# Performance work log

Hardware: AMD Instinct MI355X
Metric: run time of the kernel (lower is better)

Reference implementation:

```python
import jax, jax.numpy as jnp
import numpy as np
from jax import lax

NUM_EXPERTS = 5
K = 3


def setup_inputs() -> dict:
    key = jax.random.key(0)
    ks = jax.random.split(key, 16)
    B = 8192
    d_in, d_h = 32 * 10 * 10, 128

    def w(k, shape, fan_in):
        return jax.random.normal(k, shape, jnp.float32) / np.sqrt(fan_in)

    return {
        "x": jax.random.normal(ks[0], (B, 1, 28, 28), jnp.float32),
        # conv feature extractor: 28 -> conv5 -> 24 -> pool2 -> 12 -> conv3 -> 10
        "conv1_w": w(ks[1], (16, 1, 5, 5), 25),
        "conv1_b": jnp.zeros((16,), jnp.float32),
        "conv2_w": w(ks[2], (32, 16, 3, 3), 16 * 9),
        "conv2_b": jnp.zeros((32,), jnp.float32),
        # top-k gate
        "gate_w": w(ks[3], (d_in, NUM_EXPERTS), d_in),
        "gate_b": jnp.zeros((NUM_EXPERTS,), jnp.float32),
        # 5 experts: Linear(3200,128)-Tanh-Linear(128,128)-Tanh, stacked on axis 0
        "e1_w": w(ks[4], (NUM_EXPERTS, d_in, d_h), d_in),
        "e1_b": jnp.zeros((NUM_EXPERTS, d_h), jnp.float32),
        "e2_w": w(ks[5], (NUM_EXPERTS, d_h, d_h), d_h),
        "e2_b": jnp.zeros((NUM_EXPERTS, d_h), jnp.float32),
        # softmax head
        "sm_w": w(ks[6], (d_h, 10), d_h),
        "sm_b": jnp.zeros((10,), jnp.float32),
    }


def _conv_features(x, c1w, c1b, c2w, c2b):
    dn = ("NCHW", "OIHW", "NCHW")
    h = lax.conv_general_dilated(x, c1w, (1, 1), "VALID", dimension_numbers=dn)
    h = jax.nn.relu(h + c1b[None, :, None, None])          # [B,16,24,24]
    h = lax.reduce_window(h, -jnp.inf, lax.max, (1, 1, 2, 2), (1, 1, 2, 2), "VALID")  # [B,16,12,12]
    h = lax.conv_general_dilated(h, c2w, (1, 1), "VALID", dimension_numbers=dn)
    h = jax.nn.relu(h + c2b[None, :, None, None])          # [B,32,10,10]
    return h.reshape(h.shape[0], -1)                       # [B,3200]


def reference(x, conv1_w, conv1_b, conv2_w, conv2_b, gate_w, gate_b,
              e1_w, e1_b, e2_w, e2_b, sm_w, sm_b):
    h = _conv_features(x, conv1_w, conv1_b, conv2_w, conv2_b)  # [B, 3200]
    B = h.shape[0]

    # token-choice top-K gating over NUM_EXPERTS experts
    probs = jax.nn.softmax(h @ gate_w + gate_b, axis=-1)       # [B, E]
    topv, topi = lax.top_k(probs, K)                           # [B, K]
    topv = topv / jnp.sum(topv, axis=-1, keepdims=True)        # renormalize
    w_full = jnp.zeros((B, NUM_EXPERTS), h.dtype).at[
        jnp.arange(B)[:, None], topi].set(topv)                # [B, E] sparse combine weights

    # expert MLPs (small, computed densely and masked by gate weights)
    h1 = jnp.tanh(jnp.einsum("bd,edh->ebh", h, e1_w) + e1_b[:, None, :])   # [E,B,128]
    h2 = jnp.tanh(jnp.einsum("ebh,ehk->ebk", h1, e2_w) + e2_b[:, None, :])  # [E,B,128]
    moe_out = jnp.einsum("be,ebk->bk", w_full, h2)             # weighted sum combine, [B,128]

    logits = moe_out @ sm_w + sm_b                             # [B,10]
    return jax.nn.softmax(logits, axis=1)
```

## Files before the change

### kernel.cpp

```cpp
#include <hip/hip_runtime.h>
#include <hip/hip_bf16.h>
#include <hip/hip_fp16.h>

#define NB 8192
#define D_IN 3200
#define D_H 128
#define NE 5

typedef _Float16 f16x8 __attribute__((ext_vector_type(8)));
typedef _Float16 f16x4 __attribute__((ext_vector_type(4)));
typedef float f32x4 __attribute__((ext_vector_type(4)));

__device__ __forceinline__ void gload16(const _Float16* g, _Float16* l) {
    __builtin_amdgcn_global_load_lds(
        (const __attribute__((address_space(1))) void*)g,
        (__attribute__((address_space(3))) void*)l, 16, 0, 0);
}

__global__ __launch_bounds__(256) void k_gwprep(const float* __restrict__ gw,
                                                float* __restrict__ gwC,
                                                int* __restrict__ cnt) {
    int i = blockIdx.x * 256 + threadIdx.x;
    if (i < 16000) {
        int e = i / 3200, rem = i - e * 3200;
        int o = rem >> 5, co = rem & 31;
        gwC[i] = gw[(co * 100 + o) * 5 + e];
    }
    if (blockIdx.x == 0 && threadIdx.x < NE) cnt[threadIdx.x] = 0;
}

#define PCL_S 24
__global__ __launch_bounds__(256, 3) void k_feat(
    const float* __restrict__ x, const float* __restrict__ c1w, const float* __restrict__ c1b,
    const float* __restrict__ c2w, const float* __restrict__ c2b,
    const float* __restrict__ gwC, const float* __restrict__ gb,
    const float* __restrict__ e1w, _Float16* __restrict__ wT,
    const float* __restrict__ e2w, _Float16* __restrict__ e2T,
    _Float16* __restrict__ h16, float* __restrict__ wfull)
{
    __shared__ union {
        struct {
            __align__(16) float xs[784];
            __align__(16) float c1wsP[448];
            __align__(16) _Float16 b2h[5120];
            __align__(16) _Float16 b2l[5120];
            __align__(16) _Float16 pclh[144 * PCL_S];
            __align__(16) _Float16 pcll[144 * PCL_S];
            float red[32];
        } f;
        float tile[64 * 65];
    } S;
    int bid = blockIdx.x;
    int t = threadIdx.x;

    if (bid < 520) {
        if (bid < 500) {
            int e = bid / 100, rem = bid - e * 100;
            int k0 = (rem >> 1) * 64, n0 = (rem & 1) * 64;
            const float* src = e1w + (size_t)e * D_IN * D_H;
            _Float16* dst = wT + (size_t)e * D_H * D_IN;
            for (int i = 0; i < 16; ++i) {
                int idx = t + i * 256;
                int kr = idx >> 6, nc = idx & 63;
                S.tile[kr * 65 + nc] = src[(size_t)(k0 + kr) * D_H + n0 + nc];
            }
            __syncthreads();
            for (int i = 0; i < 16; ++i) {
                int idx = t + i * 256;
                int nr = idx >> 6, kc = idx & 63;
                dst[(size_t)(n0 + nr) * D_IN + k0 + kc] = (_Float16)S.tile[kc * 65 + nr];
            }
        } else {
            int idx2 = bid - 500;
            int e = idx2 >> 2, rem = idx2 & 3;
            int k0 = (rem >> 1) * 64, n0 = (rem & 1) * 64;
            const float* src = e2w + (size_t)e * D_H * D_H;
            _Float16* dst = e2T + (size_t)e * D_H * D_H;
            for (int i = 0; i < 16; ++i) {
                int idx = t + i * 256;
                int kr = idx >> 6, nc = idx & 63;
                S.tile[kr * 65 + nc] = src[(size_t)(k0 + kr) * D_H + n0 + nc];
            }
            __syncthreads();
            for (int i = 0; i < 16; ++i) {
                int idx = t + i * 256;
                int nr = idx >> 6, kc = idx & 63;
                dst[(size_t)(n0 + nr) * D_H + k0 + kc] = (_Float16)S.tile[kc * 65 + nr];
            }
        }
        return;
    }

    int b = bid - 520;
    for (int i = t; i < 784; i += 256) S.f.xs[i] = x[(size_t)b * 784 + i];
    for (int i = t; i < 400; i += 256) {
        int c = i / 25, q = i - c * 25;
        S.f.c1wsP[c * 28 + q] = c1w[i];
    }
    for (int i = t; i < 5120; i += 256) {
        int co = i / 160, k = i - co * 160;
        int s = k >> 4, ci = k & 15;
        float v = (s == 9) ? 0.f : c2w[(co * 16 + ci) * 9 + s];
        _Float16 vh = (_Float16)v;
        S.f.b2h[i] = vh;
        S.f.b2l[i] = (_Float16)(v - (float)vh);
    }
    __syncthreads();

    {
        int c = t >> 4;
        int tile = t & 15;
        int tr = tile >> 2, tc = tile & 3;
        float w1r[25];
        #pragma unroll
        for (int q = 0; q < 6; ++q) {
            float4 v4 = *(const float4*)&S.f.c1wsP[c * 28 + q * 4];
            w1r[q * 4 + 0] = v4.x; w1r[q * 4 + 1] = v4.y;
            w1r[q * 4 + 2] = v4.z; w1r[q * 4 + 3] = v4.w;
        }
        w1r[24] = S.f.c1wsP[c * 28 + 24];
        float bias1 = c1b[c];
        float win[5][10];
        float pacc[3][3];
        #pragma unroll
        for (int i = 0; i < 3; ++i)
            #pragma unroll
            for (int j = 0; j < 3; ++j) pacc[i][j] = 0.f;
        int r0 = 6 * tr, col0 = 6 * tc;
        #pragma unroll
        for (int cr = 0; cr < 6; ++cr) {
            if (cr == 0) {
                #pragma unroll
                for (int rr = 0; rr < 5; ++rr)
                    #pragma unroll
                    for (int m = 0; m < 5; ++m) {
                        float2 v = *(const float2*)&S.f.xs[(r0 + rr) * 28 + col0 + 2 * m];
                        win[rr][2 * m] = v.x; win[rr][2 * m + 1] = v.y;
                    }
            } else {
                int dstr = (cr + 4) % 5;
                #pragma unroll
                for (int m = 0; m < 5; ++m) {
                    float2 v = *(const float2*)&S.f.xs[(r0 + cr + 4) * 28 + col0 + 2 * m];
                    win[dstr][2 * m] = v.x; win[dstr][2 * m + 1] = v.y;
                }
            }
            #pragma unroll
            for (int oc = 0; oc < 6; ++oc) {
                float s = bias1;
                #pragma unroll
                for (int u = 0; u < 5; ++u)
                    #pragma unroll
                    for (int v = 0; v < 5; ++v)
                        s += win[(cr + u) % 5][oc + v] * w1r[u * 5 + v];
                s = fmaxf(s, 0.f);
                pacc[cr >> 1][oc >> 1] = fmaxf(pacc[cr >> 1][oc >> 1], s);
            }
        }
        #pragma unroll
        for (int i = 0; i < 3; ++i)
            #pragma unroll
            for (int j = 0; j < 3; ++j) {
                int pos = (3 * tr + i) * 12 + (3 * tc + j);
                float v = pacc[i][j];
                _Float16 vh = (_Float16)v;
                S.f.pclh[pos * PCL_S + c] = vh;
                S.f.pcll[pos * PCL_S + c] = (_Float16)(v - (float)vh);
            }
    }
    __syncthreads();

    float part[5] = {0, 0, 0, 0, 0};
    int lane = t & 63, wv = t >> 6;
    int quad = lane >> 4, l16 = lane & 15;
    int quadh = quad >> 1, quadl = quad & 1;
    const int offA[5] = {0, 2, 13, 24, 26};
    const int offB[5] = {1, 12, 14, 25, 0};
    {
        int nt = wv & 1;
        int co = nt * 16 + l16;
        f16x8 bh[5], bl[5];
        #pragma unroll
        for (int kc = 0; kc < 5; ++kc) {
            bh[kc] = *(const f16x8*)&S.f.b2h[co * 160 + kc * 32 + quad * 8];
            bl[kc] = *(const f16x8*)&S.f.b2l[co * 160 + kc * 32 + quad * 8];
        }
        float bco = c2b[co];
        for (int mt = wv >> 1; mt < 7; mt += 2) {
            int o_a = mt * 16 + l16;
            int o_cl = o_a < 100 ? o_a : 99;
            int pb = (o_cl / 10) * 12 + (o_cl % 10);
            f32x4 acc = (f32x4){0.f, 0.f, 0.f, 0.f};
            #pragma unroll
            for (int kc = 0; kc < 5; ++kc) {
                int off = quadh ? offB[kc] : offA[kc];
                f16x8 ah = *(const f16x8*)&S.f.pclh[(pb + off) * PCL_S + quadl * 8];
                f16x8 al = *(const f16x8*)&S.f.pcll[(pb + off) * PCL_S + quadl * 8];
                acc = __builtin_amdgcn_mfma_f32_16x16x32_f16(ah, bh[kc], acc, 0, 0, 0);
                acc = __builtin_amdgcn_mfma_f32_16x16x32_f16(ah, bl[kc], acc, 0, 0, 0);
                acc = __builtin_amdgcn_mfma_f32_16x16x32_f16(al, bh[kc], acc, 0, 0, 0);
            }
            if (mt < 6 || quad == 0) {
                int o0 = mt * 16 + quad * 4;
                f16x4 st;
                #pragma unroll
                for (int r = 0; r < 4; ++r) {
                    float hv = fmaxf(acc[r] + bco, 0.f);
                    st[r] = (_Float16)hv;
                    #pragma unroll
                    for (int e = 0; e < 5; ++e)
                        part[e] += hv * gwC[e * 3200 + (o0 + r) * 32 + co];
                }
                *(f16x4*)&h16[(size_t)b * D_IN + co * 100 + o0] = st;
            }
        }
    }

    #pragma unroll
    for (int e = 0; e < 5; ++e) {
        float v = part[e];
        for (int off = 32; off > 0; off >>= 1) v += __shfl_down(v, off, 64);
        if (lane == 0) S.f.red[wv * 8 + e] = v;
    }
    __syncthreads();
    if (t == 0) {
        float lg[5], p[5];
        float mx = -1e30f;
        for (int e = 0; e < 5; ++e) {
            lg[e] = S.f.red[e] + S.f.red[8 + e] + S.f.red[16 + e] + S.f.red[24 + e] + gb[e];
            mx = fmaxf(mx, lg[e]);
        }
        float sum = 0.f;
        for (int e = 0; e < 5; ++e) { p[e] = expf(lg[e] - mx); sum += p[e]; }
        for (int e = 0; e < 5; ++e) p[e] /= sum;
        bool used[5] = {false, false, false, false, false};
        float out5[5] = {0, 0, 0, 0, 0};
        int ti[3]; float tv[3]; float tsum = 0.f;
        for (int jj = 0; jj < 3; ++jj) {
            int best = 0; float bv = -1.f;
            for (int e = 0; e < 5; ++e)
                if (!used[e] && p[e] > bv) { bv = p[e]; best = e; }
            used[best] = true; ti[jj] = best; tv[jj] = bv; tsum += bv;
        }
        for (int jj = 0; jj < 3; ++jj) out5[ti[jj]] = tv[jj] / tsum;
        for (int e = 0; e < 5; ++e) wfull[b * 5 + e] = out5[e];
    }
}

__global__ __launch_bounds__(256) void k_compact(
    const float* __restrict__ wfull, int* __restrict__ cnt, int* __restrict__ lists)
{
    int tok = blockIdx.x * 256 + threadIdx.x;
    int lane = threadIdx.x & 63;
    float w[5];
    #pragma unroll
    for (int e = 0; e < 5; ++e) w[e] = wfull[(size_t)tok * 5 + e];
    #pragma unroll
    for (int e = 0; e < 5; ++e) {
        bool sel = w[e] > 0.f;
        unsigned long long mask = __ballot(sel);
        int leader = __ffsll((long long)mask) - 1;
        int base = 0;
        if (lane == leader) base = atomicAdd(&cnt[e], __popcll(mask));
        base = __shfl(base, leader, 64);
        if (sel) {
            int pos = base + __popcll(mask & ((1ull << lane) - 1ull));
            lists[e * NB + pos] = tok;
        }
    }
}

#define H1S 136
union __align__(16) SLds {
    struct { _Float16 As0[2048], As1[2048], Bs0[4096], Bs1[4096]; } p[2];
    struct {
        __align__(16) _Float16 h1s[64 * H1S];
        __align__(16) _Float16 e2ws[128 * H1S];
    } q;
};

__global__ __launch_bounds__(256, 3) void k_e1e2(
    const _Float16* __restrict__ h16, const _Float16* __restrict__ wT,
    const _Float16* __restrict__ e2T,
    const float* __restrict__ e1b, const float* __restrict__ e2b,
    const float* __restrict__ smw,
    const float* __restrict__ wfull, const int* __restrict__ cnt,
    const int* __restrict__ lists, float* __restrict__ logits)
{
    __shared__ SLds u;
    __shared__ float wfl[64];
    __shared__ int rows[64];
    int bid = blockIdx.x;
    int e = bid >> 7;
    int mt = bid & 127;
    int cnt_e = cnt[e];
    int m0 = mt * 64;
    if (m0 >= cnt_e) return;
    int t = threadIdx.x;
    int lane = t & 63, wv = t >> 6;
    int waveM = wv >> 1, waveN = wv & 1;
    int quad = lane >> 4, l16 = lane & 15;
    if (t < 64) {
        int r = m0 + t;
        int row = (r < cnt_e) ? lists[e * NB + r] : lists[e * NB];
        rows[t] = row;
        wfl[t] = (r < cnt_e) ? wfull[(size_t)row * 5 + e] : 0.f;
    }
    __syncthreads();

    const _Float16* bbase = wT + (size_t)e * (D_H * D_IN);
    int srow = t >> 2;
    int scol = (t & 3) * 8;
    const _Float16* aptr = h16 + (size_t)rows[srow] * D_IN + scol;
    const _Float16* bptr0 = bbase + (size_t)srow * D_IN + scol;
    const _Float16* bptr1 = bbase + (size_t)(64 + srow) * D_IN + scol;
    f32x4 acc[2][4];
    #pragma unroll
    for (int i = 0; i < 2; ++i)
        #pragma unroll
        for (int j = 0; j < 4; ++j) acc[i][j] = (f32x4){0.f, 0.f, 0.f, 0.f};

    _Float16* bufc = (_Float16*)&u.p[0];
    _Float16* bufn = (_Float16*)&u.p[1];
    #define STAGE(base, kk)                                           \
        do {                                                          \
            gload16(aptr  + (kk),        (base) + 0    + wv * 512);   \
            gload16(aptr  + (kk) + 32,   (base) + 2048 + wv * 512);   \
            gload16(bptr0 + (kk),        (base) + 4096 + wv * 512);   \
            gload16(bptr0 + (kk) + 32,   (base) + 8192 + wv * 512);   \
            gload16(bptr1 + (kk),        (base) + 4096 + 2048 + wv * 512); \
            gload16(bptr1 + (kk) + 32,   (base) + 8192 + 2048 + wv * 512); \
        } while (0)

    STAGE(bufc, 0);
    const int NT = D_IN / 64;
    for (int it = 0; it < NT; ++it) {
        if (it + 1 < NT) {
            STAGE(bufn, (it + 1) * 64);
            asm volatile("s_waitcnt vmcnt(6)" ::: "memory");
        } else {
            asm volatile("s_waitcnt vmcnt(0)" ::: "memory");
        }
        __builtin_amdgcn_s_barrier();
        __builtin_amdgcn_sched_barrier(0);
        #pragma unroll
        for (int ch = 0; ch < 2; ++ch) {
            const _Float16* Ab = bufc + (ch ? 2048 : 0);
            const _Float16* Bb = bufc + 4096 + (ch ? 4096 : 0);
            f16x8 af[2], bf[4];
            #pragma unroll
            for (int ms = 0; ms < 2; ++ms)
                af[ms] = *(const f16x8*)&Ab[(waveM * 32 + ms * 16 + l16) * 32 + quad * 8];
            #pragma unroll
            for (int ns = 0; ns < 4; ++ns)
                bf[ns] = *(const f16x8*)&Bb[(waveN * 64 + ns * 16 + l16) * 32 + quad * 8];
            #pragma unroll
            for (int ms = 0; ms < 2; ++ms)
                #pragma unroll
                for (int ns = 0; ns < 4; ++ns)
                    acc[ms][ns] = __builtin_amdgcn_mfma_f32_16x16x32_f16(af[ms], bf[ns], acc[ms][ns], 0, 0, 0);
        }
        __builtin_amdgcn_s_barrier();
        _Float16* tmp = bufc; bufc = bufn; bufn = tmp;
    }
    #undef STAGE

    #pragma unroll
    for (int ms = 0; ms < 2; ++ms) {
        int rbase = waveM * 32 + ms * 16 + quad * 4;
        #pragma unroll
        for (int ns = 0; ns < 4; ++ns) {
            int n = waveN * 64 + ns * 16 + l16;
            float bias = e1b[e * D_H + n];
            #pragma unroll
            for (int r = 0; r < 4; ++r)
                u.q.h1s[(rbase + r) * H1S + n] = (_Float16)tanhf(acc[ms][ns][r] + bias);
        }
    }
    __syncthreads();

    {
        int rr = t >> 1, cc = (t & 1) * 64;
        const _Float16* src = e2T + (size_t)e * (D_H * D_H) + (size_t)rr * D_H + cc;
        #pragma unroll
        for (int i = 0; i < 8; ++i)
            *(uint4*)&u.q.e2ws[rr * H1S + cc + i * 8] = *(const uint4*)(src + i * 8);
    }
    __syncthreads();

    f32x4 acc2[2][4];
    #pragma unroll
    for (int i = 0; i < 2; ++i)
        #pragma unroll
        for (int j = 0; j < 4; ++j) acc2[i][j] = (f32x4){0.f, 0.f, 0.f, 0.f};
    #pragma unroll
    for (int kc = 0; kc < 4; ++kc) {
        f16x8 a2[2], b2[4];
        #pragma unroll
        for (int ms = 0; ms < 2; ++ms)
            a2[ms] = *(const f16x8*)&u.q.h1s[(waveM * 32 + ms * 16 + l16) * H1S + kc * 32 + quad * 8];
        #pragma unroll
        for (int ns = 0; ns < 4; ++ns)
            b2[ns] = *(const f16x8*)&u.q.e2ws[(waveN * 64 + ns * 16 + l16) * H1S + kc * 32 + quad * 8];
        #pragma unroll
        for (int ms = 0; ms < 2; ++ms)
            #pragma unroll
            for (int ns = 0; ns < 4; ++ns)
                acc2[ms][ns] = __builtin_amdgcn_mfma_f32_16x16x32_f16(a2[ms], b2[ns], acc2[ms][ns], 0, 0, 0);
    }
    __syncthreads();

    _Float16* smwT = u.q.e2ws;
    for (int i = t; i < 2048; i += 256) {
        int n = i >> 7, k = i & 127;
        smwT[i] = (_Float16)(n < 10 ? smw[k * 10 + n] : 0.f);
    }
    #pragma unroll
    for (int ms = 0; ms < 2; ++ms) {
        int rbase = waveM * 32 + ms * 16 + quad * 4;
        #pragma unroll
        for (int ns = 0; ns < 4; ++ns) {
            int n = waveN * 64 + ns * 16 + l16;
            float bias = e2b[e * D_H + n];
            #pragma unroll
            for (int r = 0; r < 4; ++r) {
                int lrow = rbase + r;
                u.q.h1s[lrow * H1S + n] = (_Float16)(wfl[lrow] * tanhf(acc2[ms][ns][r] + bias));
            }
        }
    }
    __syncthreads();

    {
        f32x4 acc3 = (f32x4){0.f, 0.f, 0.f, 0.f};
        #pragma unroll
        for (int kc = 0; kc < 4; ++kc) {
            f16x8 a3 = *(const f16x8*)&u.q.h1s[(wv * 16 + l16) * H1S + kc * 32 + quad * 8];
            f16x8 b3 = *(const f16x8*)&smwT[l16 * 128 + kc * 32 + quad * 8];
            acc3 = __builtin_amdgcn_mfma_f32_16x16x32_f16(a3, b3, acc3, 0, 0, 0);
        }
        if (l16 < 10) {
            #pragma unroll
            for (int r = 0; r < 4; ++r) {
                int row = wv * 16 + quad * 4 + r;
                unsafeAtomicAdd(&logits[(size_t)rows[row] * 10 + l16], acc3[r]);
            }
        }
    }
}

__global__ __launch_bounds__(256) void k_smax(
    const float* __restrict__ logits, const float* __restrict__ smb,
    float* __restrict__ out)
{
    int r = blockIdx.x * 256 + threadIdx.x;
    float lg[10];
    float mx = -1e30f;
    #pragma unroll
    for (int c = 0; c < 10; ++c) {
        lg[c] = logits[(size_t)r * 10 + c] + smb[c];
        mx = fmaxf(mx, lg[c]);
    }
    float s = 0.f;
    #pragma unroll
    for (int c = 0; c < 10; ++c) { lg[c] = expf(lg[c] - mx); s += lg[c]; }
    float inv = 1.f / s;
    #pragma unroll
    for (int c = 0; c < 10; ++c) out[(size_t)r * 10 + c] = lg[c] * inv;
}

extern "C" void kernel_launch(void* const* d_in, const int* in_sizes, int n_in,
                              void* d_out, int out_size, void* d_ws, size_t ws_size,
                              hipStream_t stream)
{
    const float* x   = (const float*)d_in[0];
    const float* c1w = (const float*)d_in[1];
    const float* c1b = (const float*)d_in[2];
    const float* c2w = (const float*)d_in[3];
    const float* c2b = (const float*)d_in[4];
    const float* gw  = (const float*)d_in[5];
    const float* gb  = (const float*)d_in[6];
    const float* e1w = (const float*)d_in[7];
    const float* e1b = (const float*)d_in[8];
    const float* e2w = (const float*)d_in[9];
    const float* e2b = (const float*)d_in[10];
    const float* smw = (const float*)d_in[11];
    const float* smb = (const float*)d_in[12];
    float* out = (float*)d_out;

    char* ws = (char*)d_ws;
    size_t off = 0;
    auto alloc = [&](size_t bytes) {
        void* p = ws + off;
        off += (bytes + 255) & ~(size_t)255;
        return p;
    };
    _Float16* h16 = (_Float16*)alloc((size_t)NB * D_IN * 2);
    _Float16* wT  = (_Float16*)alloc((size_t)NE * D_H * D_IN * 2);
    _Float16* e2T = (_Float16*)alloc((size_t)NE * D_H * D_H * 2);
    float* wfull  = (float*)alloc((size_t)NB * NE * 4);
    float* logits = (float*)alloc((size_t)NB * 10 * 4);
    float* gwC    = (float*)alloc((size_t)NE * D_IN * 4);
    int* cnt      = (int*)alloc(NE * 4);
    int* lists    = (int*)alloc((size_t)NE * NB * 4);

    hipMemsetAsync(logits, 0, (size_t)NB * 10 * 4, stream);
    k_gwprep<<<dim3(63), 256, 0, stream>>>(gw, gwC, cnt);
    k_feat<<<dim3(520 + NB), 256, 0, stream>>>(x, c1w, c1b, c2w, c2b, gwC, gb,
                                               e1w, wT, e2w, e2T, h16, wfull);
    k_compact<<<dim3(NB / 256), 256, 0, stream>>>(wfull, cnt, lists);
    k_e1e2<<<dim3(128 * NE), 256, 0, stream>>>(h16, wT, e2T, e1b, e2b, smw,
                                               wfull, cnt, lists, logits);
    k_smax<<<dim3(NB / 256), 256, 0, stream>>>(logits, smb, out);
}
```

Measured before the change: 304.8 us.

## Run conv1 on MFMA with split-fp16 and precompute packed conv weights

Conv1 plus maxpool moves from a scalar FP32 sliding-window loop to MFMA 16x16x32 f16 instructions. Inputs and weights are split into hi/lo fp16 pairs and three MFMAs per tile recover near-fp32 accuracy. The conv2 and conv1 weight split/packing now happens once in the prep kernel, and each block copies the packed weights into LDS with direct global-to-LDS loads instead of recomputing them per block. LDS use shrinks enough that launch bounds rise to 4 blocks per SM, at some accuracy risk from dropping the lo*lo term.

```diff
diff --git a/kernel.cpp b/kernel.cpp
--- a/kernel.cpp
+++ b/kernel.cpp
@@ -17,33 +17,63 @@
         (__attribute__((address_space(3))) void*)l, 16, 0, 0);
 }
 
-__global__ __launch_bounds__(256) void k_gwprep(const float* __restrict__ gw,
-                                                float* __restrict__ gwC,
-                                                int* __restrict__ cnt) {
+__device__ __forceinline__ unsigned pack_hl(float v) {
+    _Float16 vh = (_Float16)v;
+    _Float16 vl = (_Float16)(v - (float)vh);
+    unsigned short uh, ul;
+    __builtin_memcpy(&uh, &vh, 2);
+    __builtin_memcpy(&ul, &vl, 2);
+    return (unsigned)uh | ((unsigned)ul << 16);
+}
+
+__global__ __launch_bounds__(256) void k_prep(const float* __restrict__ gw,
+                                              const float* __restrict__ c2w,
+                                              const float* __restrict__ c1w,
+                                              float* __restrict__ gwC,
+                                              _Float16* __restrict__ wpk,
+                                              int* __restrict__ cnt) {
     int i = blockIdx.x * 256 + threadIdx.x;
     if (i < 16000) {
         int e = i / 3200, rem = i - e * 3200;
         int o = rem >> 5, co = rem & 31;
         gwC[i] = gw[(co * 100 + o) * 5 + e];
+    } else if (i < 21120) {
+        int j = i - 16000;
+        int co = j / 160, k = j - co * 160;
+        int s = k >> 4, ci = k & 15;
+        float v = (s == 9) ? 0.f : c2w[(co * 16 + ci) * 9 + s];
+        _Float16 vh = (_Float16)v;
+        wpk[j] = vh;
+        wpk[5120 + j] = (_Float16)(v - (float)vh);
+    } else if (i < 21760) {
+        int j = i - 21120;
+        int c = (j * 1639) >> 16;
+        int k = j - c * 40;
+        float v = (k < 25) ? c1w[c * 25 + k] : 0.f;
+        _Float16 vh = (_Float16)v;
+        wpk[10240 + j] = vh;
+        wpk[10880 + j] = (_Float16)(v - (float)vh);
     }
     if (blockIdx.x == 0 && threadIdx.x < NE) cnt[threadIdx.x] = 0;
 }
 
 #define PCL_S 24
-__global__ __launch_bounds__(256, 3) void k_feat(
-    const float* __restrict__ x, const float* __restrict__ c1w, const float* __restrict__ c1b,
-    const float* __restrict__ c2w, const float* __restrict__ c2b,
+__global__ __launch_bounds__(256, 4) void k_feat(
+    const float* __restrict__ x, const float* __restrict__ c1b,
+    const float* __restrict__ c2b,
     const float* __restrict__ gwC, const float* __restrict__ gb,
+    const _Float16* __restrict__ wpk,
     const float* __restrict__ e1w, _Float16* __restrict__ wT,
     const float* __restrict__ e2w, _Float16* __restrict__ e2T,
     _Float16* __restrict__ h16, float* __restrict__ wfull)
 {
     __shared__ union {
         struct {
-            __align__(16) float xs[784];
-            __align__(16) float c1wsP[448];
             __align__(16) _Float16 b2h[5120];
             __align__(16) _Float16 b2l[5120];
+            __align__(16) _Float16 b1h[640];
+            __align__(16) _Float16 b1l[640];
+            __align__(16) unsigned xs_hl[784];
             __align__(16) _Float16 pclh[144 * PCL_S];
             __align__(16) _Float16 pcll[144 * PCL_S];
             float red[32];
@@ -92,87 +122,63 @@
     }
 
     int b = bid - 520;
-    for (int i = t; i < 784; i += 256) S.f.xs[i] = x[(size_t)b * 784 + i];
-    for (int i = t; i < 400; i += 256) {
-        int c = i / 25, q = i - c * 25;
-        S.f.c1wsP[c * 28 + q] = c1w[i];
-    }
-    for (int i = t; i < 5120; i += 256) {
-        int co = i / 160, k = i - co * 160;
-        int s = k >> 4, ci = k & 15;
-        float v = (s == 9) ? 0.f : c2w[(co * 16 + ci) * 9 + s];
-        _Float16 vh = (_Float16)v;
-        S.f.b2h[i] = vh;
-        S.f.b2l[i] = (_Float16)(v - (float)vh);
-    }
-    __syncthreads();
-
-    {
-        int c = t >> 4;
-        int tile = t & 15;
-        int tr = tile >> 2, tc = tile & 3;
-        float w1r[25];
-        #pragma unroll
-        for (int q = 0; q < 6; ++q) {
-            float4 v4 = *(const float4*)&S.f.c1wsP[c * 28 + q * 4];
-            w1r[q * 4 + 0] = v4.x; w1r[q * 4 + 1] = v4.y;
-            w1r[q * 4 + 2] = v4.z; w1r[q * 4 + 3] = v4.w;
-        }
-        w1r[24] = S.f.c1wsP[c * 28 + 24];
-        float bias1 = c1b[c];
-        float win[5][10];
-        float pacc[3][3];
-        #pragma unroll
-        for (int i = 0; i < 3; ++i)
-            #pragma unroll
-            for (int j = 0; j < 3; ++j) pacc[i][j] = 0.f;
-        int r0 = 6 * tr, col0 = 6 * tc;
-        #pragma unroll
-        for (int cr = 0; cr < 6; ++cr) {
-            if (cr == 0) {
-                #pragma unroll
-                for (int rr = 0; rr < 5; ++rr)
-                    #pragma unroll
-                    for (int m = 0; m < 5; ++m) {
-                        float2 v = *(const float2*)&S.f.xs[(r0 + rr) * 28 + col0 + 2 * m];
-                        win[rr][2 * m] = v.x; win[rr][2 * m + 1] = v.y;
-                    }
-            } else {
-                int dstr = (cr + 4) % 5;
-                #pragma unroll
-                for (int m = 0; m < 5; ++m) {
-                    float2 v = *(const float2*)&S.f.xs[(r0 + cr + 4) * 28 + col0 + 2 * m];
-                    win[dstr][2 * m] = v.x; win[dstr][2 * m + 1] = v.y;
-                }
-            }
-            #pragma unroll
-            for (int oc = 0; oc < 6; ++oc) {
-                float s = bias1;
-                #pragma unroll
-                for (int u = 0; u < 5; ++u)
-                    #pragma unroll
-                    for (int v = 0; v < 5; ++v)
-                        s += win[(cr + u) % 5][oc + v] * w1r[u * 5 + v];
-                s = fmaxf(s, 0.f);
-                pacc[cr >> 1][oc >> 1] = fmaxf(pacc[cr >> 1][oc >> 1], s);
-            }
-        }
-        #pragma unroll
-        for (int i = 0; i < 3; ++i)
-            #pragma unroll
-            for (int j = 0; j < 3; ++j) {
-                int pos = (3 * tr + i) * 12 + (3 * tc + j);
-                float v = pacc[i][j];
-                _Float16 vh = (_Float16)v;
-                S.f.pclh[pos * PCL_S + c] = vh;
-                S.f.pcll[pos * PCL_S + c] = (_Float16)(v - (float)vh);
-            }
-    }
-    __syncthreads();
-
-    float part[5] = {0, 0, 0, 0, 0};
     int lane = t & 63, wv = t >> 6;
     int quad = lane >> 4, l16 = lane & 15;
+
+    {
+        _Float16* ldst = S.f.b2h;
+        #pragma unroll
+        for (int it = 0; it < 6; ++it) {
+            int ci = t + it * 256;
+            if (ci < 1440)
+                gload16(wpk + ci * 8, ldst + (it * 256 + wv * 64) * 8);
+        }
+    }
+    for (int i = t; i < 784; i += 256)
+        S.f.xs_hl[i] = pack_hl(x[(size_t)b * 784 + i]);
+    __syncthreads();
+
+    {
+        f16x8 b1hf = *(const f16x8*)&S.f.b1h[l16 * 40 + quad * 8];
+        f16x8 b1lf = *(const f16x8*)&S.f.b1l[l16 * 40 + quad * 8];
+        float bias1 = c1b[l16];
+        int offw[8];
+        #pragma unroll
+        for (int j = 0; j < 8; ++j) {
+            int k = quad * 8 + j; if (k > 24) k = 24;
+            int uu = (k * 205) >> 10;
+            offw[j] = k + 23 * uu;
+        }
+        int s_ = l16 & 3, qof = l16 >> 2;
+        int dy = s_ >> 1, dx = s_ & 1;
+        for (int T = wv * 9; T < wv * 9 + 9; ++T) {
+            int q = T * 4 + qof;
+            int qy = (q * 683) >> 13, qx = q - qy * 12;
+            int base = (2 * qy + dy) * 28 + 2 * qx + dx;
+            unsigned w[8];
+            #pragma unroll
+            for (int j = 0; j < 8; ++j) w[j] = S.f.xs_hl[base + offw[j]];
+            union { f16x8 v; unsigned u[4]; } ah, al;
+            #pragma unroll
+            for (int jj = 0; jj < 4; ++jj) {
+                ah.u[jj] = __builtin_amdgcn_perm(w[2 * jj + 1], w[2 * jj], 0x05040100u);
+                al.u[jj] = __builtin_amdgcn_perm(w[2 * jj + 1], w[2 * jj], 0x07060302u);
+            }
+            f32x4 a1 = (f32x4){0.f, 0.f, 0.f, 0.f};
+            a1 = __builtin_amdgcn_mfma_f32_16x16x32_f16(ah.v, b1hf, a1, 0, 0, 0);
+            a1 = __builtin_amdgcn_mfma_f32_16x16x32_f16(ah.v, b1lf, a1, 0, 0, 0);
+            a1 = __builtin_amdgcn_mfma_f32_16x16x32_f16(al.v, b1hf, a1, 0, 0, 0);
+            float pv = fmaxf(fmaxf(a1[0], a1[1]), fmaxf(a1[2], a1[3]));
+            pv = fmaxf(pv + bias1, 0.f);
+            int pos = T * 4 + quad;
+            _Float16 vh = (_Float16)pv;
+            S.f.pclh[pos * PCL_S + l16] = vh;
+            S.f.pcll[pos * PCL_S + l16] = (_Float16)(pv - (float)vh);
+        }
+    }
+    __syncthreads();
+
+    float part[5] = {0, 0, 0, 0, 0};
     int quadh = quad >> 1, quadl = quad & 1;
     const int offA[5] = {0, 2, 13, 24, 26};
     const int offB[5] = {1, 12, 14, 25, 0};
@@ -501,12 +507,13 @@
     float* wfull  = (float*)alloc((size_t)NB * NE * 4);
     float* logits = (float*)alloc((size_t)NB * 10 * 4);
     float* gwC    = (float*)alloc((size_t)NE * D_IN * 4);
+    _Float16* wpk = (_Float16*)alloc((size_t)11520 * 2);
     int* cnt      = (int*)alloc(NE * 4);
     int* lists    = (int*)alloc((size_t)NE * NB * 4);
 
     hipMemsetAsync(logits, 0, (size_t)NB * 10 * 4, stream);
-    k_gwprep<<<dim3(63), 256, 0, stream>>>(gw, gwC, cnt);
-    k_feat<<<dim3(520 + NB), 256, 0, stream>>>(x, c1w, c1b, c2w, c2b, gwC, gb,
+    k_prep<<<dim3(85), 256, 0, stream>>>(gw, c2w, c1w, gwC, wpk, cnt);
+    k_feat<<<dim3(520 + NB), 256, 0, stream>>>(x, c1b, c2b, gwC, gb, wpk,
                                                e1w, wT, e2w, e2T, h16, wfull);
     k_compact<<<dim3(NB / 256), 256, 0, stream>>>(wfull, cnt, lists);
     k_e1e2<<<dim3(128 * NE), 256, 0, stream>>>(h16, wT, e2T, e1b, e2b, smw,
```

Result: faster. 264.1 us (-13.4%).
